# Kernel tuning notes

Measured on AMD Instinct MI355X. Metric: run time of the kernel, lower is better.

Reference implementation:

```python
import jax, jax.numpy as jnp
import numpy as np

F_DIM = 128
N_NODES = 2000
N_EDGES = 64000
BATCH = 4
NUM_NEG = 32
NUM_REL = 18
NUM_LAYERS = 3
NODE_RATIO = 0.1
AVG_DEG_LOG = float(np.log(33.0))  # PNA scaler constant (avg in-degree ~32); source used a ones(1) placeholder which yields inf
EPS_STD = 1e-5
NEG_BIG = -1e30


def setup_inputs() -> dict:
    key = jax.random.key(0)
    ks = jax.random.split(key, 24)
    F = F_DIM

    def W(k, fin, fout):
        return jax.random.normal(k, (fin, fout), jnp.float32) / np.float32(np.sqrt(fin))

    return {
        "h_index": jax.random.randint(ks[0], (BATCH, NUM_NEG), 0, N_NODES),
        "r_index": jax.random.randint(ks[1], (BATCH, NUM_NEG), 0, NUM_REL),
        "t_index": jax.random.randint(ks[2], (BATCH, NUM_NEG), 0, N_NODES),
        "hidden_states": jax.random.normal(ks[3], (BATCH, F), jnp.float32),
        "rel_hidden_states": jax.random.normal(ks[4], (BATCH, F), jnp.float32),
        "edge_index": jax.random.randint(ks[5], (2, N_EDGES), 0, N_NODES),
        "x": jax.random.normal(ks[6], (N_NODES, F), jnp.float32),
        "batch": jnp.zeros((N_NODES,), jnp.int32),
        "rel_table": jax.random.normal(ks[7], (2 * NUM_REL, F), jnp.float32) * 0.1,
        "Wl": W(ks[8], 2 * F, F), "bl": jnp.zeros((F,), jnp.float32),
        "W1": W(ks[9], F, F), "b1": jnp.zeros((F,), jnp.float32),
        "W2": W(ks[10], F, 1), "b2": jnp.zeros((1,), jnp.float32),
        "Wpre": jnp.stack([W(ks[11 + i], 2 * F, F) for i in range(NUM_LAYERS)]),
        "bpre": jnp.zeros((NUM_LAYERS, F), jnp.float32),
        "Wpost": jnp.stack([W(ks[14 + i], 13 * F, F) for i in range(NUM_LAYERS)]),
        "bpost": jnp.zeros((NUM_LAYERS, F), jnp.float32),
        "Wlin": jnp.stack([W(ks[17 + i], F, F) for i in range(NUM_LAYERS)]),
        "blin": jnp.zeros((NUM_LAYERS, F), jnp.float32),
    }


def _score(hidden, rel, Wl, bl, W1, b1, W2, b2):
    # ConditionedPNA.score: heur = Linear(cat[hidden, rel]); mlp(heur * hidden).squeeze(-1)
    heur = jnp.concatenate([hidden, rel], -1) @ Wl + bl
    z = heur * hidden
    z = jax.nn.relu(z @ W1 + b1)
    return (z @ W2 + b2)[..., 0]


def _pna_conv(xn, row, col, emask, Wpre, bpre, Wpost, bpost, Wlin, blin):
    # PyG PNAConv, towers=1, pre/post_layers=1, aggr=[mean,max,min,std], scalers=[id,amp,att].
    # Edge subset (topk-selected edges with degree_ratio=1.0) expressed as boolean mask emask.
    Nn = xn.shape[0]
    m = jnp.concatenate([xn[col], xn[row]], -1) @ Wpre + bpre  # [E, F] message = pre_nn(cat[x_i, x_j])
    w = emask.astype(xn.dtype)
    cnt = jax.ops.segment_sum(w, col, Nn)                       # in-degree of masked subgraph
    denom = jnp.maximum(cnt, 1.0)[:, None]
    mw = m * w[:, None]
    mean = jax.ops.segment_sum(mw, col, Nn) / denom
    mean2 = jax.ops.segment_sum(m * mw, col, Nn) / denom
    std = jnp.sqrt(jax.nn.relu(mean2 - mean * mean) + EPS_STD)
    has = cnt[:, None] > 0
    mx = jnp.where(has, jax.ops.segment_max(jnp.where(emask[:, None], m, NEG_BIG), col, Nn), 0.0)
    mn = jnp.where(has, jax.ops.segment_min(jnp.where(emask[:, None], m, -NEG_BIG), col, Nn), 0.0)
    agg = jnp.concatenate([mean, mx, mn, std], -1)              # [Nn, 4F]
    logd = jnp.log(jnp.maximum(cnt, 1.0) + 1.0)[:, None]
    out = jnp.concatenate([agg, agg * (logd / AVG_DEG_LOG), agg * (AVG_DEG_LOG / logd)], -1)  # [Nn, 12F]
    h = jnp.concatenate([xn, out], -1) @ Wpost + bpost          # post_nn on cat[x, out]
    return h @ Wlin + blin


def reference(h_index, r_index, t_index, hidden_states, rel_hidden_states, edge_index, x, batch,
              rel_table, Wl, bl, W1, b1, W2, b2, Wpre, bpre, Wpost, bpost, Wlin, blin):
    B = h_index.shape[0]
    N, F = x.shape
    # negative_sample_to_tail
    is_t = jnp.all(h_index == h_index[:, :1], axis=-1, keepdims=True)
    h_idx = jnp.where(is_t, h_index, t_index)
    t_idx = jnp.where(is_t, t_index, h_index)
    r_idx = jnp.where(is_t, r_index, r_index + NUM_REL)
    rel_emb = rel_table[r_idx[:, 0]]  # [B, F]
    # repeat_graph
    offsets = (jnp.arange(B) * N).astype(h_idx.dtype)
    row = (edge_index[0][None, :] + offsets[:, None]).reshape(-1)  # [B*E]
    col = (edge_index[1][None, :] + offsets[:, None]).reshape(-1)
    h_idx = h_idx + offsets[:, None]
    t_idx = t_idx + offsets[:, None]
    Nn = B * N
    # init_input_embeds (x zeroed, then t then h written)
    xr = jnp.zeros((Nn, F), x.dtype)
    xr = xr.at[t_idx[:, 0]].set(rel_hidden_states)
    xr = xr.at[h_idx[:, 0]].set(hidden_states)
    s0 = jnp.zeros((Nn,), x.dtype).at[h_idx[:, 0]].set(
        _score(hidden_states, rel_emb, Wl, bl, W1, b1, W2, b2))
    score = jnp.repeat(s0, N)  # faithful repeat_interleave -> length B*N*N
    rel_exp = jnp.repeat(rel_emb, N, axis=0)  # [B*N, F]
    cur = xr
    for l in range(NUM_LAYERS):
        # select_edges: topk nodes by score, keep edges whose source is selected (degree_ratio=1.0)
        k = int(NODE_RATIO * score.shape[0])
        _, top_idx = jax.lax.top_k(score, k)
        node_sel = jnp.zeros((score.shape[0],), jnp.bool_).at[top_idx].set(True)
        emask = node_sel[row]
        cur = cur + _pna_conv(cur, row, col, emask,
                              Wpre[l], bpre[l], Wpost[l], bpost[l], Wlin[l], blin[l])
        score = _score(cur, rel_exp, Wl, bl, W1, b1, W2, b2)  # [B*N]
    return score[t_idx]  # [B, num_neg]
```

## Files before the change

### kernel.cpp

```cpp
#include <hip/hip_runtime.h>

#define F 128
#define NNODE 2000
#define NEDGE 64000
#define NBATCH 4
#define NN 8000
#define NRELC 18
#define KTOP 800
#define AVGLOG 3.4965075614664802f
#define EPSSTD 1e-5f
#define NCHUNK 250


__global__ void k_init(float* __restrict__ cur, int* __restrict__ hist){
  int i = blockIdx.x*blockDim.x + threadIdx.x;
  int stride = gridDim.x*blockDim.x;
  for(int t=i;t<NN*F;t+=stride) cur[t]=0.f;
  for(int t=i;t<NCHUNK*NNODE;t+=stride) hist[t]=0;
}

__global__ void k_meta(const int* __restrict__ h_index, const int* __restrict__ r_index,
                       const int* __restrict__ t_index, const float* __restrict__ hidden,
                       const float* __restrict__ rel_hidden, const float* __restrict__ rel_table,
                       const float* __restrict__ Wl, const float* __restrict__ bl,
                       const float* __restrict__ W1, const float* __restrict__ b1,
                       const float* __restrict__ W2, const float* __restrict__ b2,
                       float* __restrict__ cur, unsigned char* __restrict__ sel,
                       int* __restrict__ meta_i, float* __restrict__ meta_f){
  __shared__ int sh_ist[NBATCH], sh_h0[NBATCH], sh_t0[NBATCH], sh_r0[NBATCH];
  __shared__ float sh_rel[NBATCH*F];
  __shared__ float sh_z[F], sh_zz[F];
  __shared__ float sh_sc[NBATCH];
  __shared__ int sh_excl;
  int tid = threadIdx.x;
  if(tid<NBATCH){
    int b=tid;
    int h00=h_index[b*32];
    int ist=1;
    for(int j=1;j<32;j++) if(h_index[b*32+j]!=h00) ist=0;
    sh_ist[b]=ist;
    sh_h0[b] = (ist ? h_index[b*32] : t_index[b*32]) + b*NNODE;
    sh_t0[b] = (ist ? t_index[b*32] : h_index[b*32]) + b*NNODE;
    sh_r0[b] = r_index[b*32] + (ist?0:NRELC);
  }
  __syncthreads();
  if(tid<NBATCH*32){
    int b=tid>>5;
    meta_i[16+tid] = (sh_ist[b] ? t_index[tid] : h_index[tid]) + b*NNODE;
  }
  for(int t=tid;t<NBATCH*F;t+=blockDim.x){
    int b=t>>7, f=t&127;
    float v = rel_table[sh_r0[b]*F+f];
    sh_rel[t]=v; meta_f[t]=v;
  }
  __syncthreads();
  for(int t=tid;t<NBATCH*F;t+=blockDim.x){
    int b=t>>7, f=t&127;
    float acc=0.f;
    for(int k=0;k<F;k++) acc += sh_rel[b*F+k]*Wl[(F+k)*F+f];
    meta_f[512+t]=acc;
  }
  __syncthreads();
  for(int b=0;b<NBATCH;b++){
    if(tid<F){
      float acc=0.f;
      for(int k=0;k<F;k++) acc += hidden[b*F+k]*Wl[k*F+tid];
      float heur = acc + meta_f[512+b*F+tid] + bl[tid];
      sh_z[tid] = heur*hidden[b*F+tid];
    }
    __syncthreads();
    if(tid<F){
      float acc=0.f;
      for(int k=0;k<F;k++) acc += sh_z[k]*W1[k*F+tid];
      acc += b1[tid];
      sh_zz[tid] = acc>0.f?acc:0.f;
    }
    __syncthreads();
    if(tid==0){
      float s=0.f;
      for(int k=0;k<F;k++) s += sh_zz[k]*W2[k];
      sh_sc[b] = s + b2[0];
      meta_f[1024+b]=sh_sc[b];
    }
    __syncthreads();
  }
  if(tid==0){
    sh_excl = (sh_h0[0]<4 && sh_sc[0]<0.f) ? sh_h0[0] : -1;
    meta_i[8]=sh_excl;
  }
  __syncthreads();
  int ex = sh_excl;
  for(int t=tid;t<NN;t+=blockDim.x)
    sel[t] = (ex>=0 && (t/NNODE)==ex) ? 0 : 1;
  for(int t=tid;t<NBATCH*F;t+=blockDim.x){
    int b=t>>7, f=t&127;
    cur[sh_t0[b]*F+f] = rel_hidden[t];
  }
  __syncthreads();
  for(int t=tid;t<NBATCH*F;t+=blockDim.x){
    int b=t>>7, f=t&127;
    cur[sh_h0[b]*F+f] = hidden[t];
  }
}

__global__ __launch_bounds__(256) void k_hist(const int* __restrict__ edge,
                                              int* __restrict__ hist, int* __restrict__ rank){
  __shared__ int dsts[256];
  int chunk = blockIdx.x;
  int tid = threadIdx.x;
  int e = chunk*256 + tid;
  int d = edge[NEDGE + e];
  dsts[tid] = d;
  __syncthreads();
  int before=0, after=0;
  #pragma unroll 8
  for(int t=0;t<256;t++){
    int dt = dsts[t];
    before += (dt==d) & (t<tid);
    after  += (dt==d) & (t>tid);
  }
  rank[e] = before;
  if(after==0) hist[chunk*NNODE + d] = before+1;
}

__global__ void k_chunkscan(int* __restrict__ hist, int* __restrict__ deg){
  int node = blockIdx.x*blockDim.x + threadIdx.x;
  if(node>=NNODE) return;
  int run=0;
  for(int c=0;c<NCHUNK;c++){
    int v = hist[c*NNODE+node];
    hist[c*NNODE+node] = run;
    run += v;
  }
  deg[node]=run;
}

__global__ void k_scan(const int* __restrict__ deg, int* __restrict__ csr_start){
  __shared__ int a[2048], b[2048];
  int tid=threadIdx.x;
  for(int i=tid;i<2048;i+=256) a[i] = (i<NNODE)? deg[i] : 0;
  __syncthreads();
  int* src=a; int* dst=b;
  for(int off=1; off<2048; off<<=1){
    for(int i=tid;i<2048;i+=256){
      int v = src[i];
      if(i>=off) v += src[i-off];
      dst[i]=v;
    }
    __syncthreads();
    int* t=src; src=dst; dst=t;
  }
  for(int i=tid;i<=NNODE;i+=256) csr_start[i] = (i==0)?0:src[i-1];
}

__global__ void k_scatter(const int* __restrict__ edge, const int* __restrict__ hist,
                          const int* __restrict__ rank, const int* __restrict__ csr_start,
                          int* __restrict__ csr_src){
  int e = blockIdx.x*blockDim.x + threadIdx.x;
  if(e<NEDGE){
    int d = edge[NEDGE+e];
    int pos = csr_start[d] + hist[(e>>8)*NNODE + d] + rank[e];
    csr_src[pos] = edge[e];
  }
}


__global__ void k_sel(const float* __restrict__ score, unsigned char* __restrict__ sel){
  __shared__ float s[NN];
  int tid=threadIdx.x;
  float4* s4 = (float4*)s;
  const float4* g4 = (const float4*)score;
  for(int i=tid;i<NN/4;i+=256) s4[i]=g4[i];
  __syncthreads();
  int node = blockIdx.x*32 + (tid>>3);
  int part = tid & 7;
  float si = s[node];
  int rank = 0;
  for(int q=part*(NN/32); q<(part+1)*(NN/32); q++){
    float4 v = s4[q];
    int j = q*4;
    rank += (v.x>si)||(v.x==si && j  <node);
    rank += (v.y>si)||(v.y==si && j+1<node);
    rank += (v.z>si)||(v.z==si && j+2<node);
    rank += (v.w>si)||(v.w==si && j+3<node);
  }
  for(int o=4;o;o>>=1) rank += __shfl_down(rank, o, 8);
  if(part==0) sel[node] = (rank < KTOP) ? 1 : 0;
}

template<int MODE>
__global__ __launch_bounds__(256) void k_gemm(
    const float* __restrict__ A, const float* __restrict__ W,
    const float* __restrict__ bias, float* __restrict__ out,
    const float* __restrict__ AGGp, const float* __restrict__ F1p,
    const float* __restrict__ F2p, const float* __restrict__ CURp, int Ktot)
{
  __shared__ float As[2][32][36];
  __shared__ float Bs[2][32][132];
  int tid = threadIdx.x;
  int r0 = blockIdx.x*32;
  int nblk = blockIdx.y*128;
  int w  = tid>>6;
  int ml = (tid&63)>>3;
  int nl = tid&7;
  int am  = tid>>3;
  int ak4 = (tid&7)*4;
  int bk  = (tid>>5)*4;
  int bc  = (tid&31)*4;

  float mul1=1.f, mul2=1.f;
  if(MODE==1){ mul1 = F1p[r0+am]; mul2 = F2p[r0+am]; }

  float4 pa; float pmult=1.f; float4 pb[4];
  int nt = Ktot/32;

  auto load_tile = [&](int t){
    int k0 = t*32;
    const float* src; float mult = 1.f;
    if(MODE==1){
      if(k0<F)          src = CURp + (size_t)(r0+am)*F   + k0;
      else if(k0<640)   src = AGGp + (size_t)(r0+am)*512 + (k0-F);
      else if(k0<1152){ src = AGGp + (size_t)(r0+am)*512 + (k0-640);  mult=mul1; }
      else            { src = AGGp + (size_t)(r0+am)*512 + (k0-1152); mult=mul2; }
    } else src = A + (size_t)(r0+am)*F + k0;
    pa = *(const float4*)(src + ak4);
    pmult = mult;
    #pragma unroll
    for(int jj=0;jj<4;jj++){
      int wr = k0 + bk + jj, wc = nblk + bc;
      if(MODE==0 && nblk>=F){ wr+=F; wc-=F; }
      pb[jj] = *(const float4*)&W[(size_t)wr*F + wc];
    }
  };
  auto store_tile = [&](int b){
    float4 v = pa;
    if(MODE==1){ v.x*=pmult; v.y*=pmult; v.z*=pmult; v.w*=pmult; }
    As[b][ak4  ][am] = v.x;
    As[b][ak4+1][am] = v.y;
    As[b][ak4+2][am] = v.z;
    As[b][ak4+3][am] = v.w;
    #pragma unroll
    for(int jj=0;jj<4;jj++)
      *(float4*)&Bs[b][bk+jj][bc] = pb[jj];
  };

  float acc[4][4]={};
  load_tile(0);
  store_tile(0);
  __syncthreads();
  for(int t=0;t<nt;t++){
    if(t+1<nt) load_tile(t+1);
    int b = t&1;
    #pragma unroll
    for(int k=0;k<32;k++){
      float4 av = *(const float4*)&As[b][k][4*ml];
      float4 bv = *(const float4*)&Bs[b][k][32*w + 4*nl];
      float ax[4] = {av.x, av.y, av.z, av.w};
      #pragma unroll
      for(int i=0;i<4;i++){
        acc[i][0] += ax[i]*bv.x;
        acc[i][1] += ax[i]*bv.y;
        acc[i][2] += ax[i]*bv.z;
        acc[i][3] += ax[i]*bv.w;
      }
    }
    if(t+1<nt) store_tile((t+1)&1);
    __syncthreads();
  }

  int cc0 = 32*w + 4*nl;
  #pragma unroll
  for(int i=0;i<4;i++){
    int rr = r0 + 4*ml + i;
    if(MODE==0){
      int cg = nblk + cc0;
      float4 o;
      if(nblk < F){
        o.x = acc[i][0]+bias[cc0  ]; o.y = acc[i][1]+bias[cc0+1];
        o.z = acc[i][2]+bias[cc0+2]; o.w = acc[i][3]+bias[cc0+3];
      } else {
        o.x = acc[i][0]; o.y = acc[i][1]; o.z = acc[i][2]; o.w = acc[i][3];
      }
      *(float4*)&out[(size_t)rr*256 + cg] = o;
    } else {
      float4 o;
      o.x = acc[i][0]+bias[cc0  ]; o.y = acc[i][1]+bias[cc0+1];
      o.z = acc[i][2]+bias[cc0+2]; o.w = acc[i][3]+bias[cc0+3];
      *(float4*)&out[(size_t)rr*F + cc0] = o;
    }
  }
}

__global__ __launch_bounds__(256) void k_tail(
    const float* __restrict__ Hb, float* __restrict__ cur,
    const float* __restrict__ Wlin, const float* __restrict__ blin,
    const float* __restrict__ Wl, const float* __restrict__ bl,
    const float* __restrict__ W1, const float* __restrict__ b1,
    const float* __restrict__ W2, const float* __restrict__ b2,
    const float* __restrict__ RB, float* __restrict__ score)
{
  __shared__ float At [128][34];
  __shared__ float At2[128][34];
  __shared__ float Bs [32][128];
  int tid = threadIdx.x;
  int r0 = blockIdx.x*32;
  int tm4 = (tid>>5)*4;
  int tn4 = (tid&31)*4;
  int am  = tid>>3;
  int ak4 = (tid&7)*4;
  int bk  = (tid>>5)*4;
  int bc  = (tid&31)*4;

  #pragma unroll
  for(int kb=0;kb<4;kb++){
    float4 v = *(const float4*)&Hb[(size_t)(r0+am)*F + kb*32 + ak4];
    At[kb*32+ak4  ][am] = v.x;
    At[kb*32+ak4+1][am] = v.y;
    At[kb*32+ak4+2][am] = v.z;
    At[kb*32+ak4+3][am] = v.w;
  }
  __syncthreads();

  float acc[4][4];

  #pragma unroll
  for(int i=0;i<4;i++) for(int j=0;j<4;j++) acc[i][j]=0.f;
  for(int kt=0;kt<4;kt++){
    #pragma unroll
    for(int jj=0;jj<4;jj++)
      *(float4*)&Bs[bk+jj][bc] = *(const float4*)&Wlin[(size_t)(kt*32+bk+jj)*F + bc];
    __syncthreads();
    #pragma unroll
    for(int k=0;k<32;k++){
      float2 alo = *(const float2*)&At[kt*32+k][tm4];
      float2 ahi = *(const float2*)&At[kt*32+k][tm4+2];
      float4 bv  = *(const float4*)&Bs[k][tn4];
      float av[4] = {alo.x, alo.y, ahi.x, ahi.y};
      #pragma unroll
      for(int i=0;i<4;i++){
        acc[i][0]+=av[i]*bv.x; acc[i][1]+=av[i]*bv.y;
        acc[i][2]+=av[i]*bv.z; acc[i][3]+=av[i]*bv.w;
      }
    }
    __syncthreads();
  }
  #pragma unroll
  for(int i=0;i<4;i++){
    int rr = r0 + tm4 + i;
    float4 c4 = *(const float4*)&cur[(size_t)rr*F + tn4];
    float cv[4] = {c4.x, c4.y, c4.z, c4.w};
    float ov[4];
    #pragma unroll
    for(int j=0;j<4;j++){
      int cc = tn4 + j;
      float val = cv[j] + (acc[i][j] + blin[cc]);
      ov[j] = val;
      At2[cc][tm4+i] = val;
    }
    float4 o4 = {ov[0],ov[1],ov[2],ov[3]};
    *(float4*)&cur[(size_t)rr*F + tn4] = o4;
  }
  __syncthreads();

  #pragma unroll
  for(int i=0;i<4;i++) for(int j=0;j<4;j++) acc[i][j]=0.f;
  for(int kt=0;kt<4;kt++){
    #pragma unroll
    for(int jj=0;jj<4;jj++)
      *(float4*)&Bs[bk+jj][bc] = *(const float4*)&Wl[(size_t)(kt*32+bk+jj)*F + bc];
    __syncthreads();
    #pragma unroll
    for(int k=0;k<32;k++){
      float2 alo = *(const float2*)&At2[kt*32+k][tm4];
      float2 ahi = *(const float2*)&At2[kt*32+k][tm4+2];
      float4 bv  = *(const float4*)&Bs[k][tn4];
      float av[4] = {alo.x, alo.y, ahi.x, ahi.y};
      #pragma unroll
      for(int i=0;i<4;i++){
        acc[i][0]+=av[i]*bv.x; acc[i][1]+=av[i]*bv.y;
        acc[i][2]+=av[i]*bv.z; acc[i][3]+=av[i]*bv.w;
      }
    }
    __syncthreads();
  }
  #pragma unroll
  for(int i=0;i<4;i++){
    int rr = r0 + tm4 + i;
    int bidx = rr/NNODE;
    #pragma unroll
    for(int j=0;j<4;j++){
      int cc = tn4 + j;
      float h = acc[i][j] + bl[cc] + RB[bidx*F+cc];
      float z = h * At2[cc][tm4+i];
      At[cc][tm4+i] = z;
    }
  }
  __syncthreads();

  #pragma unroll
  for(int i=0;i<4;i++) for(int j=0;j<4;j++) acc[i][j]=0.f;
  for(int kt=0;kt<4;kt++){
    #pragma unroll
    for(int jj=0;jj<4;jj++)
      *(float4*)&Bs[bk+jj][bc] = *(const float4*)&W1[(size_t)(kt*32+bk+jj)*F + bc];
    __syncthreads();
    #pragma unroll
    for(int k=0;k<32;k++){
      float2 alo = *(const float2*)&At[kt*32+k][tm4];
      float2 ahi = *(const float2*)&At[kt*32+k][tm4+2];
      float4 bv  = *(const float4*)&Bs[k][tn4];
      float av[4] = {alo.x, alo.y, ahi.x, ahi.y};
      #pragma unroll
      for(int i=0;i<4;i++){
        acc[i][0]+=av[i]*bv.x; acc[i][1]+=av[i]*bv.y;
        acc[i][2]+=av[i]*bv.z; acc[i][3]+=av[i]*bv.w;
      }
    }
    __syncthreads();
  }
  #pragma unroll
  for(int i=0;i<4;i++){
    #pragma unroll
    for(int j=0;j<4;j++){
      int cc = tn4 + j;
      float h = acc[i][j] + b1[cc];
      At2[cc][tm4+i] = h>0.f ? h : 0.f;
    }
  }
  __syncthreads();

  int wv = tid>>6, ln = tid&63;
  for(int r8=0;r8<8;r8++){
    int r = wv*8 + r8;
    float zx = At2[2*ln  ][r];
    float zy = At2[2*ln+1][r];
    float p = zx*W2[ln*2] + zy*W2[ln*2+1];
    for(int o=32;o;o>>=1) p += __shfl_down(p,o);
    if(ln==0) score[r0+r] = p + b2[0];
  }
}

__global__ void k_agg(const float* __restrict__ AB, const unsigned char* __restrict__ sel,
                      const int* __restrict__ csr_start, const int* __restrict__ csr_src,
                      float* __restrict__ AGGo, float* __restrict__ F1o, float* __restrict__ F2o){
  int node = blockIdx.x*4 + (threadIdx.x>>6);
  int lane = threadIdx.x&63;
  int b = node/NNODE;
  int nl = node - b*NNODE;
  int boff = b*NNODE;
  int e0=csr_start[nl], e1=csr_start[nl+1];
  int f0=lane*2;
  float2 c = *(const float2*)&AB[(size_t)node*256 + f0];
  float s1x=0,s1y=0,s2x=0,s2y=0;
  float mxx=-3e38f,mxy=-3e38f,mnx=3e38f,mny=3e38f;
  int cnt=0;
  for(int base=e0;base<e1;base+=64){
    int nch = e1-base; if(nch>64) nch=64;
    int pack=-1;
    if(lane<nch){
      int sg = csr_src[base+lane]+boff;
      pack = sel[sg] ? sg : -1;
    }
    for(int t=0;t<nch;t++){
      int sg = __shfl(pack, t);
      if(sg>=0){
        float2 v = *(const float2*)&AB[(size_t)sg*256 + F + f0];
        float ma = c.x+v.x, mb = c.y+v.y;
        s1x+=ma; s1y+=mb;
        s2x+=ma*ma; s2y+=mb*mb;
        mxx=fmaxf(mxx,ma); mxy=fmaxf(mxy,mb);
        mnx=fminf(mnx,ma); mny=fminf(mny,mb);
        cnt++;
      }
    }
  }
  float meanx,meany,stdx,stdy,mxox,mxoy,mnox,mnoy;
  if(cnt>0){
    float fc=(float)cnt;
    meanx=s1x/fc; meany=s1y/fc;
    float m2x=s2x/fc, m2y=s2y/fc;
    float vx=m2x-meanx*meanx; if(vx<0.f)vx=0.f;
    float vy=m2y-meany*meany; if(vy<0.f)vy=0.f;
    stdx=sqrtf(vx+EPSSTD); stdy=sqrtf(vy+EPSSTD);
    mxox=mxx; mxoy=mxy; mnox=mnx; mnoy=mny;
  } else {
    meanx=0.f; meany=0.f;
    stdx=sqrtf(EPSSTD); stdy=stdx;
    mxox=0.f; mxoy=0.f; mnox=0.f; mnoy=0.f;
  }
  float logd = logf(fmaxf((float)cnt,1.f)+1.f);
  float2 w0={meanx,meany}; *(float2*)&AGGo[(size_t)node*512      +f0]=w0;
  float2 w1={mxox,mxoy};   *(float2*)&AGGo[(size_t)node*512+F    +f0]=w1;
  float2 w2v={mnox,mnoy};  *(float2*)&AGGo[(size_t)node*512+2*F  +f0]=w2v;
  float2 w3={stdx,stdy};   *(float2*)&AGGo[(size_t)node*512+3*F  +f0]=w3;
  if(lane==0){ F1o[node]=logd/AVGLOG; F2o[node]=AVGLOG/logd; }
}

__global__ void k_gather(const float* __restrict__ score, const int* __restrict__ meta_i,
                         float* __restrict__ outp){
  int t = threadIdx.x;
  if(t<128) outp[t] = score[meta_i[16+t]];
}


extern "C" void kernel_launch(void* const* d_in, const int* in_sizes, int n_in,
                              void* d_out, int out_size, void* d_ws, size_t ws_size,
                              hipStream_t stream){
  const int*   h_index    = (const int*)d_in[0];
  const int*   r_index    = (const int*)d_in[1];
  const int*   t_index    = (const int*)d_in[2];
  const float* hidden     = (const float*)d_in[3];
  const float* rel_hidden = (const float*)d_in[4];
  const int*   edge       = (const int*)d_in[5];
  const float* rel_table  = (const float*)d_in[8];
  const float* Wl =(const float*)d_in[9];   const float* bl =(const float*)d_in[10];
  const float* W1 =(const float*)d_in[11];  const float* b1 =(const float*)d_in[12];
  const float* W2 =(const float*)d_in[13];  const float* b2 =(const float*)d_in[14];
  const float* Wpre =(const float*)d_in[15];  const float* bpre =(const float*)d_in[16];
  const float* Wpost=(const float*)d_in[17];  const float* bpost=(const float*)d_in[18];
  const float* Wlin =(const float*)d_in[19];  const float* blin =(const float*)d_in[20];

  char* ws=(char*)d_ws;
  size_t off=0;
  auto alloc=[&](size_t bytes)->char*{ char* p=ws+off; off=(off+bytes+255)&~(size_t)255; return p; };
  float* cur   =(float*)alloc((size_t)NN*F*4);
  float* AB    =(float*)alloc((size_t)NN*256*4);
  float* AGG   =(float*)alloc((size_t)NN*512*4);
  float* Hb    =(float*)alloc((size_t)NN*F*4);
  float* score =(float*)alloc((size_t)NN*4);
  float* F1b   =(float*)alloc((size_t)NN*4);
  float* F2b   =(float*)alloc((size_t)NN*4);
  float* meta_f=(float*)alloc(2048*4);
  int*   meta_i=(int*)alloc(256*4);
  int*   deg   =(int*)alloc(NNODE*4);
  int*   csr_start=(int*)alloc((NNODE+1)*4);
  int*   csr_src  =(int*)alloc((size_t)NEDGE*4);
  int*   hist  =(int*)alloc((size_t)NCHUNK*NNODE*4);
  int*   rank  =(int*)alloc((size_t)NEDGE*4);
  unsigned char* sel=(unsigned char*)alloc(NN);

  k_init<<<512,256,0,stream>>>(cur, hist);
  k_meta<<<1,256,0,stream>>>(h_index,r_index,t_index,hidden,rel_hidden,rel_table,
                             Wl,bl,W1,b1,W2,b2,cur,sel,meta_i,meta_f);
  k_hist<<<NCHUNK,256,0,stream>>>(edge, hist, rank);
  k_chunkscan<<<8,256,0,stream>>>(hist, deg);
  k_scan<<<1,256,0,stream>>>(deg, csr_start);
  k_scatter<<<250,256,0,stream>>>(edge, hist, rank, csr_start, csr_src);

  for(int l=0;l<3;l++){
    if(l) k_sel<<<250,256,0,stream>>>(score, sel);
    k_gemm<0><<<dim3(250,2),256,0,stream>>>(cur, Wpre+(size_t)l*256*F, bpre+l*F, AB,
                                            nullptr,nullptr,nullptr,nullptr, F);
    k_agg<<<2000,256,0,stream>>>(AB, sel, csr_start, csr_src, AGG, F1b, F2b);
    k_gemm<1><<<dim3(250,1),256,0,stream>>>(nullptr, Wpost+(size_t)l*1664*F, bpost+l*F, Hb,
                                            AGG, F1b, F2b, cur, 1664);
    k_tail<<<250,256,0,stream>>>(Hb, cur, Wlin+(size_t)l*F*F, blin+l*F,
                                 Wl, bl, W1, b1, W2, b2, meta_f+512, score);
  }
  k_gather<<<1,128,0,stream>>>(score, meta_i, (float*)d_out);
}
```

Measured before the change: 748.1 us.

## Replace shared-memory tiled GEMM with register-only direct-load GEMM

The GEMM kernel no longer stages A and W tiles through shared memory with barriers. Each thread now loads its own 4 rows of A and a 4-column slice of W straight from global memory into registers, double-buffered in software. The PNA post-GEMM is split into four K segments, each applying its own scaler multiplier. This removes LDS traffic and __syncthreads, but drops cross-thread reuse, so many more global and L2 reads are issued for the same data.

```diff
diff --git a/kernel.cpp b/kernel.cpp
--- a/kernel.cpp
+++ b/kernel.cpp
@@ -188,6 +188,40 @@
   if(part==0) sel[node] = (rank < KTOP) ? 1 : 0;
 }
 
+
+#define RELOAD(AA,BB,tt){ int kq=(tt)*4; \
+  AA[0]=*(const float4*)(Ab0 + kq); \
+  AA[1]=*(const float4*)(Ab0 + (size_t)lda + kq); \
+  AA[2]=*(const float4*)(Ab0 + 2*(size_t)lda + kq); \
+  AA[3]=*(const float4*)(Ab0 + 3*(size_t)lda + kq); \
+  BB[0]=*(const float4*)(Wseg + (size_t)(kq  )*F); \
+  BB[1]=*(const float4*)(Wseg + (size_t)(kq+1)*F); \
+  BB[2]=*(const float4*)(Wseg + (size_t)(kq+2)*F); \
+  BB[3]=*(const float4*)(Wseg + (size_t)(kq+3)*F); }
+
+#define CONSUME(AA,BB,tnext){ \
+  float4 a0=AA[0],a1=AA[1],a2=AA[2],a3=AA[3]; \
+  float4 b0=BB[0],b1=BB[1],b2=BB[2],b3=BB[3]; \
+  if((tnext)<nt) RELOAD(AA,BB,tnext); \
+  if(dm){ a0.x*=m0;a0.y*=m0;a0.z*=m0;a0.w*=m0; a1.x*=m1;a1.y*=m1;a1.z*=m1;a1.w*=m1; \
+          a2.x*=m2;a2.y*=m2;a2.z*=m2;a2.w*=m2; a3.x*=m3;a3.y*=m3;a3.z*=m3;a3.w*=m3; } \
+  acc[0][0]+=a0.x*b0.x; acc[0][1]+=a0.x*b0.y; acc[0][2]+=a0.x*b0.z; acc[0][3]+=a0.x*b0.w; \
+  acc[1][0]+=a1.x*b0.x; acc[1][1]+=a1.x*b0.y; acc[1][2]+=a1.x*b0.z; acc[1][3]+=a1.x*b0.w; \
+  acc[2][0]+=a2.x*b0.x; acc[2][1]+=a2.x*b0.y; acc[2][2]+=a2.x*b0.z; acc[2][3]+=a2.x*b0.w; \
+  acc[3][0]+=a3.x*b0.x; acc[3][1]+=a3.x*b0.y; acc[3][2]+=a3.x*b0.z; acc[3][3]+=a3.x*b0.w; \
+  acc[0][0]+=a0.y*b1.x; acc[0][1]+=a0.y*b1.y; acc[0][2]+=a0.y*b1.z; acc[0][3]+=a0.y*b1.w; \
+  acc[1][0]+=a1.y*b1.x; acc[1][1]+=a1.y*b1.y; acc[1][2]+=a1.y*b1.z; acc[1][3]+=a1.y*b1.w; \
+  acc[2][0]+=a2.y*b1.x; acc[2][1]+=a2.y*b1.y; acc[2][2]+=a2.y*b1.z; acc[2][3]+=a2.y*b1.w; \
+  acc[3][0]+=a3.y*b1.x; acc[3][1]+=a3.y*b1.y; acc[3][2]+=a3.y*b1.z; acc[3][3]+=a3.y*b1.w; \
+  acc[0][0]+=a0.z*b2.x; acc[0][1]+=a0.z*b2.y; acc[0][2]+=a0.z*b2.z; acc[0][3]+=a0.z*b2.w; \
+  acc[1][0]+=a1.z*b2.x; acc[1][1]+=a1.z*b2.y; acc[1][2]+=a1.z*b2.z; acc[1][3]+=a1.z*b2.w; \
+  acc[2][0]+=a2.z*b2.x; acc[2][1]+=a2.z*b2.y; acc[2][2]+=a2.z*b2.z; acc[2][3]+=a2.z*b2.w; \
+  acc[3][0]+=a3.z*b2.x; acc[3][1]+=a3.z*b2.y; acc[3][2]+=a3.z*b2.z; acc[3][3]+=a3.z*b2.w; \
+  acc[0][0]+=a0.w*b3.x; acc[0][1]+=a0.w*b3.y; acc[0][2]+=a0.w*b3.z; acc[0][3]+=a0.w*b3.w; \
+  acc[1][0]+=a1.w*b3.x; acc[1][1]+=a1.w*b3.y; acc[1][2]+=a1.w*b3.z; acc[1][3]+=a1.w*b3.w; \
+  acc[2][0]+=a2.w*b3.x; acc[2][1]+=a2.w*b3.y; acc[2][2]+=a2.w*b3.z; acc[2][3]+=a2.w*b3.w; \
+  acc[3][0]+=a3.w*b3.x; acc[3][1]+=a3.w*b3.y; acc[3][2]+=a3.w*b3.z; acc[3][3]+=a3.w*b3.w; }
+
 template<int MODE>
 __global__ __launch_bounds__(256) void k_gemm(
     const float* __restrict__ A, const float* __restrict__ W,
@@ -195,85 +229,47 @@
     const float* __restrict__ AGGp, const float* __restrict__ F1p,
     const float* __restrict__ F2p, const float* __restrict__ CURp, int Ktot)
 {
-  __shared__ float As[2][32][36];
-  __shared__ float Bs[2][32][132];
   int tid = threadIdx.x;
   int r0 = blockIdx.x*32;
   int nblk = blockIdx.y*128;
   int w  = tid>>6;
   int ml = (tid&63)>>3;
   int nl = tid&7;
-  int am  = tid>>3;
-  int ak4 = (tid&7)*4;
-  int bk  = (tid>>5)*4;
-  int bc  = (tid&31)*4;
-
-  float mul1=1.f, mul2=1.f;
-  if(MODE==1){ mul1 = F1p[r0+am]; mul2 = F2p[r0+am]; }
-
-  float4 pa; float pmult=1.f; float4 pb[4];
-  int nt = Ktot/32;
-
-  auto load_tile = [&](int t){
-    int k0 = t*32;
-    const float* src; float mult = 1.f;
-    if(MODE==1){
-      if(k0<F)          src = CURp + (size_t)(r0+am)*F   + k0;
-      else if(k0<640)   src = AGGp + (size_t)(r0+am)*512 + (k0-F);
-      else if(k0<1152){ src = AGGp + (size_t)(r0+am)*512 + (k0-640);  mult=mul1; }
-      else            { src = AGGp + (size_t)(r0+am)*512 + (k0-1152); mult=mul2; }
-    } else src = A + (size_t)(r0+am)*F + k0;
-    pa = *(const float4*)(src + ak4);
-    pmult = mult;
-    #pragma unroll
-    for(int jj=0;jj<4;jj++){
-      int wr = k0 + bk + jj, wc = nblk + bc;
-      if(MODE==0 && nblk>=F){ wr+=F; wc-=F; }
-      pb[jj] = *(const float4*)&W[(size_t)wr*F + wc];
+  int cc0 = 32*w + 4*nl;
+  int row = r0 + 4*ml;
+
+  const float* Wcol = W + cc0 + (size_t)((MODE==0 && nblk>=F) ? F*F : 0);
+  float acc[4][4]={};
+
+  auto seg = [&](const float* Ab0, int lda, int nk,
+                 float m0, float m1, float m2, float m3,
+                 const float* Wseg, int dm){
+    int nt = nk/4;
+    float4 Pa[4],Pb[4],Qa[4],Qb[4];
+    RELOAD(Pa,Pb,0);
+    RELOAD(Qa,Qb,1);
+    for(int t=0;t<nt;t+=2){
+      CONSUME(Pa,Pb,t+2);
+      CONSUME(Qa,Qb,t+3);
     }
   };
-  auto store_tile = [&](int b){
-    float4 v = pa;
-    if(MODE==1){ v.x*=pmult; v.y*=pmult; v.z*=pmult; v.w*=pmult; }
-    As[b][ak4  ][am] = v.x;
-    As[b][ak4+1][am] = v.y;
-    As[b][ak4+2][am] = v.z;
-    As[b][ak4+3][am] = v.w;
-    #pragma unroll
-    for(int jj=0;jj<4;jj++)
-      *(float4*)&Bs[b][bk+jj][bc] = pb[jj];
-  };
-
-  float acc[4][4]={};
-  load_tile(0);
-  store_tile(0);
-  __syncthreads();
-  for(int t=0;t<nt;t++){
-    if(t+1<nt) load_tile(t+1);
-    int b = t&1;
-    #pragma unroll
-    for(int k=0;k<32;k++){
-      float4 av = *(const float4*)&As[b][k][4*ml];
-      float4 bv = *(const float4*)&Bs[b][k][32*w + 4*nl];
-      float ax[4] = {av.x, av.y, av.z, av.w};
-      #pragma unroll
-      for(int i=0;i<4;i++){
-        acc[i][0] += ax[i]*bv.x;
-        acc[i][1] += ax[i]*bv.y;
-        acc[i][2] += ax[i]*bv.z;
-        acc[i][3] += ax[i]*bv.w;
-      }
-    }
-    if(t+1<nt) store_tile((t+1)&1);
-    __syncthreads();
-  }
-
-  int cc0 = 32*w + 4*nl;
+
+  if(MODE==0){
+    seg(A + (size_t)row*F, F, Ktot, 1.f,1.f,1.f,1.f, Wcol, 0);
+  } else {
+    float f10=F1p[row], f11=F1p[row+1], f12=F1p[row+2], f13=F1p[row+3];
+    float f20=F2p[row], f21=F2p[row+1], f22=F2p[row+2], f23=F2p[row+3];
+    const float* Ag = AGGp + (size_t)row*512;
+    seg(CURp + (size_t)row*F, F, 128, 1.f,1.f,1.f,1.f, Wcol, 0);
+    seg(Ag, 512, 512, 1.f,1.f,1.f,1.f, Wcol + (size_t)128*F, 0);
+    seg(Ag, 512, 512, f10,f11,f12,f13, Wcol + (size_t)640*F, 1);
+    seg(Ag, 512, 512, f20,f21,f22,f23, Wcol + (size_t)1152*F, 1);
+  }
+
   #pragma unroll
   for(int i=0;i<4;i++){
-    int rr = r0 + 4*ml + i;
+    int rr = row + i;
     if(MODE==0){
-      int cg = nblk + cc0;
       float4 o;
       if(nblk < F){
         o.x = acc[i][0]+bias[cc0  ]; o.y = acc[i][1]+bias[cc0+1];
@@ -281,7 +277,7 @@
       } else {
         o.x = acc[i][0]; o.y = acc[i][1]; o.z = acc[i][2]; o.w = acc[i][3];
       }
-      *(float4*)&out[(size_t)rr*256 + cg] = o;
+      *(float4*)&out[(size_t)rr*256 + nblk + cc0] = o;
     } else {
       float4 o;
       o.x = acc[i][0]+bias[cc0  ]; o.y = acc[i][1]+bias[cc0+1];
```

Measured after the change: 716.8 us. 4.2% less time.
